# Kernel optimization log

Measured on AMD Instinct MI355X. Metric: run time of the kernel, lower is better.

## Reference

```python
import jax, jax.numpy as jnp
import numpy as np
import math

B, H, W = 8, 512, 1024
BOUNDARY_WIDTH = 4
BOUNDARY_ITERATION = 4
KERNEL_SIZE = 7
DILATION_SIZE = 6
NEG = -1e30  # geodesic border for morphological dilation (kornia border_type='geodesic')
POS = 1e30   # geodesic border for erosion
DN = ('NCHW', 'OIHW', 'NCHW')


def _gaussian_kernel():
    size, sigma = 7, 1.0
    g = np.fromfunction(
        lambda x, y: 1.0 / (2 * math.pi * sigma ** 2)
        * math.e ** (-(((x - (size - 1) / 2) ** 2 + (y - (size - 1) / 2) ** 2) / (2 * sigma ** 2))),
        (size, size))
    g = g / g.sum()
    return jnp.asarray(g, jnp.float32)[None, None]  # [1,1,7,7]


def _cross_dilate(x):
    # morphological dilation with 3x3 cross structuring element (generate_binary_structure(2,1))
    p = jnp.pad(x, ((0, 0), (0, 0), (1, 1), (1, 1)), constant_values=NEG)
    c = p[..., 1:-1, 1:-1]
    return jnp.maximum(
        jnp.maximum(jnp.maximum(c, p[..., :-2, 1:-1]), p[..., 2:, 1:-1]),
        jnp.maximum(p[..., 1:-1, :-2], p[..., 1:-1, 2:]))


def _erode3(x):
    # morphological erosion with full 3x3 ones structuring element, geodesic border
    return jax.lax.reduce_window(x, jnp.float32(POS), jax.lax.min,
                                 (1, 1, 3, 3), (1, 1, 1, 1),
                                 [(0, 0), (0, 0), (1, 1), (1, 1)])


def _conv3_sum(x):
    # 3x3 all-ones conv (first_conv), VALID on already-padded input
    k = jnp.ones((1, 1, 3, 3), x.dtype)
    return jax.lax.conv_general_dilated(x, k, (1, 1), 'VALID', dimension_numbers=DN)


def _forward(x, prediction):
    lab = prediction.astype(jnp.float32)
    # boundaries where dilated labels differ from eroded labels
    boundaries = (_cross_dilate(lab) != _erode3(lab)).astype(jnp.float32)
    out = x
    diff = BOUNDARY_WIDTH // BOUNDARY_ITERATION
    for it in range(BOUNDARY_ITERATION):
        prev = out
        r = 0 if (BOUNDARY_WIDTH == 0 or it == BOUNDARY_ITERATION - 1) else BOUNDARY_WIDTH - diff * it - 1
        eb = boundaries
        for _ in range(r):  # dilation by diamond of radius r == r cross-dilations
            eb = _cross_dilate(eb)
        mask = (eb == 0).astype(jnp.float32)  # non-boundary mask
        xm = out * mask
        xp = jnp.pad(xm, ((0, 0), (0, 0), (1, 1), (1, 1)), mode='edge')       # ReplicationPad2d(1)
        mp = jnp.pad(mask, ((0, 0), (0, 0), (1, 1), (1, 1)), mode='edge')
        y = _conv3_sum(xp)
        n = _conv3_sum(mp).astype(jnp.int32)  # .long() truncation; values are exact small ints
        n_safe = jnp.where(n == 0, 1, n).astype(y.dtype)
        avg = jnp.where(n == 0, prev, y / n_safe)
        out = jnp.where(mask == 0, avg, prev)
    # dilated gaussian smoothing: ReplicationPad2d(18) + 7x7 conv, dilation 6
    pad = DILATION_SIZE * 3
    op = jnp.pad(out, ((0, 0), (0, 0), (pad, pad), (pad, pad)), mode='edge')
    out = jax.lax.conv_general_dilated(op, _gaussian_kernel(), (1, 1), 'VALID',
                                       rhs_dilation=(DILATION_SIZE, DILATION_SIZE),
                                       dimension_numbers=DN)
    return out


def setup_inputs() -> dict:
    key = jax.random.key(0)
    k1, k2 = jax.random.split(key)
    x = jax.random.normal(k1, (B, 1, H, W), dtype=jnp.float32)
    prediction = jax.random.randint(k2, (B, 1, H, W), 0, 19, dtype=jnp.int32)
    return {"x": x, "prediction": prediction}


def reference(x, prediction):
    return _forward(x, prediction)
```

## Files before the change

### kernel.cpp

```cpp
#include <hip/hip_runtime.h>

#define B_ 8
#define H_ 512
#define W_ 1024
#define NPX (B_*H_*W_)

#define TILE 32
#define HD 4
#define RD 40
#define HB 7
#define RB 46
#define HP 8
#define RP 48

__device__ __forceinline__ int clampi(int v, int lo, int hi) {
    return v < lo ? lo : (v > hi ? hi : v);
}
__device__ __forceinline__ int imax(int a, int b) { return a > b ? a : b; }
__device__ __forceinline__ int imin(int a, int b) { return a < b ? a : b; }

__global__ __launch_bounds__(256)
void bsws_stage1(const float* __restrict__ xg, const int* __restrict__ predg,
                 float* __restrict__ outg)
{
    __shared__ int sPred[RP * RP];
    __shared__ unsigned long long sB[4][RB];
    __shared__ int sFlag;
    __shared__ float sA[RD * RD];
    __shared__ float sC[RD * RD];
    __shared__ float sHX[RD * RD];
    __shared__ float sHM[RD * RD];

    const int tid = threadIdx.x;
    const int x0 = blockIdx.x * TILE;
    const int y0 = blockIdx.y * TILE;
    const size_t plane = (size_t)H_ * W_;
    const int*   pp = predg + blockIdx.z * plane;
    const float* xp = xg    + blockIdx.z * plane;
    float*       op = outg  + blockIdx.z * plane;

    const bool leftB  = (x0 == 0), rightB = (x0 + TILE == W_);
    const bool topB   = (y0 == 0), botB   = (y0 + TILE == H_);
    const bool borderB = leftB || rightB || topB || botB;

    if (!borderB) {
        for (int i = tid; i < (RP * RP) / 4; i += 256) {
            int ry = i / (RP / 4);
            int c4 = i - ry * (RP / 4);
            int gy = y0 - HP + ry;
            int4 v = *(const int4*)(pp + (size_t)gy * W_ + (x0 - HP) + 4 * c4);
            *(int4*)&sPred[ry * RP + 4 * c4] = v;
        }
    } else {
        for (int i = tid; i < RP * RP; i += 256) {
            int ry = i / RP, rx = i - ry * RP;
            int gy = y0 - HP + ry, gx = x0 - HP + rx;
            sPred[i] = (gy >= 0 && gy < H_ && gx >= 0 && gx < W_) ? pp[(size_t)gy * W_ + gx] : -1;
        }
    }
    __syncthreads();

    {
        const int lane = tid & 63, wv = tid >> 6;
        for (int row = wv; row < RB; row += 4) {
            bool pred = false;
            if (lane < RB) {
                const int py = row + 1, px = lane + 1;
                int c = sPred[py * RP + px];
                if (c >= 0) {
                    int up = sPred[(py - 1) * RP + px];
                    int dn = sPred[(py + 1) * RP + px];
                    int lf = sPred[py * RP + px - 1];
                    int rt = sPred[py * RP + px + 1];
                    int ul = sPred[(py - 1) * RP + px - 1];
                    int ur = sPred[(py - 1) * RP + px + 1];
                    int dl = sPred[(py + 1) * RP + px - 1];
                    int dr = sPred[(py + 1) * RP + px + 1];
                    int mx = imax(imax(up, dn), imax(lf, rt));
                    int Bv = 0x7fffffff;
                    int mn = imin(imin(imin(up < 0 ? Bv : up, dn < 0 ? Bv : dn),
                                       imin(lf < 0 ? Bv : lf, rt < 0 ? Bv : rt)),
                                  imin(imin(ul < 0 ? Bv : ul, ur < 0 ? Bv : ur),
                                       imin(dl < 0 ? Bv : dl, dr < 0 ? Bv : dr)));
                    pred = (mx > c) || (mn < c);
                }
            }
            unsigned long long bal = __ballot(pred);
            if (lane == 0) sB[0][row] = bal;
        }
    }
    __syncthreads();

    if (tid < 64) {
        bool ok = true;
        if (tid < RB) {
            int gy = y0 - HB + tid;
            if (gy >= 0 && gy < H_) {
                int jlo = leftB ? HB : 0;
                int jhi = rightB ? (RB - 1 - HB) : (RB - 1);
                unsigned long long vmask = (((1ULL << (jhi - jlo + 1)) - 1ULL) << jlo);
                ok = ((sB[0][tid] & vmask) == vmask);
            }
        }
        unsigned long long all = __ballot(ok);
        if (tid == 0) sFlag = (all == ~0ULL) ? 1 : 0;
    }
    __syncthreads();

    if (sFlag) {
        int ty = tid >> 3, tx4 = (tid & 7) * 4;
        const float4 v = *(const float4*)(xp + (size_t)(y0 + ty) * W_ + (x0 + tx4));
        *(float4*)(op + (size_t)(y0 + ty) * W_ + (x0 + tx4)) = v;
        return;
    }

    for (int i = tid; i < RD * RD; i += 256) {
        int ry = i / RD, rx = i - ry * RD;
        int gy = clampi(y0 - HD + ry, 0, H_ - 1);
        int gx = clampi(x0 - HD + rx, 0, W_ - 1);
        sA[i] = xp[(size_t)gy * W_ + gx];
    }

    #pragma unroll
    for (int lvl = 1; lvl < 4; ++lvl) {
        __syncthreads();
        if (tid < RB) {
            unsigned long long c = sB[lvl - 1][tid];
            unsigned long long u = (tid > 0)      ? sB[lvl - 1][tid - 1] : 0ULL;
            unsigned long long d = (tid < RB - 1) ? sB[lvl - 1][tid + 1] : 0ULL;
            sB[lvl][tid] = c | (c << 1) | (c >> 1) | u | d;
        }
    }
    __syncthreads();

    if (borderB) {
        const bool act = tid < 4 * RB;
        unsigned long long val = 0; int lvl = 0, row = 0;
        if (act) {
            lvl = tid / RB; row = tid - lvl * RB;
            int srcRow = clampi(row, topB ? HB : 0, botB ? (RB - 1 - HB) : RB - 1);
            val = sB[lvl][srcRow];
            if (leftB) {
                unsigned long long b = (val >> HB) & 1ULL;
                unsigned long long lo = (1ULL << HB) - 1;
                val = (val & ~lo) | (b ? lo : 0ULL);
            }
            if (rightB) {
                const int jb = RB - 1 - HB;
                unsigned long long b = (val >> jb) & 1ULL;
                unsigned long long keep = (1ULL << (jb + 1)) - 1;
                unsigned long long hi = (((1ULL << RB) - 1) & ~keep);
                val = (val & keep) | (b ? hi : 0ULL);
            }
        }
        __syncthreads();
        if (act) sB[lvl][row] = val;
    }
    __syncthreads();

    float* cur = sA;
    float* nxt = sC;
    #pragma unroll
    for (int it = 0; it < 4; ++it) {
        const int r = 3 - it;
        const unsigned long long* br = sB[r];

        for (int i = tid; i < RD * RD; i += 256) {
            int ry = i / RD, rx = i - ry * RD;
            unsigned long long row = br[ry + (HB - HD)];
            int rxm = rx > 0 ? rx - 1 : 0;
            int rxp = rx < RD - 1 ? rx + 1 : RD - 1;
            float m0 = ((row >> (rx + 2)) & 1ULL) ? 0.f : 1.f;
            float m1 = ((row >> (rx + 3)) & 1ULL) ? 0.f : 1.f;
            float m2 = ((row >> (rx + 4)) & 1ULL) ? 0.f : 1.f;
            float a0 = cur[ry * RD + rxm];
            float a1 = cur[ry * RD + rx];
            float a2 = cur[ry * RD + rxp];
            sHX[i] = m0 * a0 + m1 * a1 + m2 * a2;
            sHM[i] = m0 + m1 + m2;
        }
        __syncthreads();

        for (int i = tid; i < 38 * 38; i += 256) {
            int q = i / 38;
            int ry = 1 + q, rx = 1 + (i - q * 38);
            int idx = ry * RD + rx;
            float n = sHM[idx - RD] + sHM[idx] + sHM[idx + RD];
            float y = sHX[idx - RD] + sHX[idx] + sHX[idx + RD];
            float c = cur[idx];
            unsigned long long row = br[ry + (HB - HD)];
            bool masked = ((row >> (rx + 3)) & 1ULL) != 0ULL;
            float avg = y * __builtin_amdgcn_rcpf(n);
            nxt[idx] = (masked && n > 0.5f) ? avg : c;
        }
        __syncthreads();

        if (borderB) {
            for (int i = tid; i < RD * RD; i += 256) {
                int ry = i / RD, rx = i - ry * RD;
                int ryc = clampi(ry, topB ? HD : 0, botB ? (RD - 1 - HD) : RD - 1);
                int rxc = clampi(rx, leftB ? HD : 0, rightB ? (RD - 1 - HD) : RD - 1);
                if (ryc != ry || rxc != rx) nxt[i] = nxt[ryc * RD + rxc];
            }
        }
        __syncthreads();
        float* t = cur; cur = nxt; nxt = t;
    }

    for (int i = tid; i < TILE * TILE; i += 256) {
        int ty = i >> 5, tx = i & 31;
        op[(size_t)(y0 + ty) * W_ + (x0 + tx)] = cur[(ty + HD) * RD + (tx + HD)];
    }
}

#define GW0 0.39905027965f
#define GW1 0.24203622800f
#define GW2 0.05400558260f
#define GW3 0.00443304810f

__global__ __launch_bounds__(256)
void gaussH(const float* __restrict__ in, float* __restrict__ out)
{
    int idx = blockIdx.x * 256 + threadIdx.x;
    const float* row = in + (idx & ~(W_ - 1));
    int gx = idx & (W_ - 1);
    float acc = GW3 * (row[clampi(gx - 18, 0, W_ - 1)] + row[clampi(gx + 18, 0, W_ - 1)])
              + GW2 * (row[clampi(gx - 12, 0, W_ - 1)] + row[clampi(gx + 12, 0, W_ - 1)])
              + GW1 * (row[clampi(gx - 6,  0, W_ - 1)] + row[clampi(gx + 6,  0, W_ - 1)])
              + GW0 *  row[gx];
    out[idx] = acc;
}

__global__ __launch_bounds__(256)
void gaussV(const float* __restrict__ in, float* __restrict__ out)
{
    int idx = blockIdx.x * 256 + threadIdx.x;
    int gx = idx & (W_ - 1);
    int gy = (idx >> 10) & (H_ - 1);
    const float* pl = in + (size_t)(idx >> 19 << 19);
    float acc = GW3 * (pl[(clampi(gy - 18, 0, H_ - 1) << 10) | gx] + pl[(clampi(gy + 18, 0, H_ - 1) << 10) | gx])
              + GW2 * (pl[(clampi(gy - 12, 0, H_ - 1) << 10) | gx] + pl[(clampi(gy + 12, 0, H_ - 1) << 10) | gx])
              + GW1 * (pl[(clampi(gy - 6,  0, H_ - 1) << 10) | gx] + pl[(clampi(gy + 6,  0, H_ - 1) << 10) | gx])
              + GW0 *  pl[(gy << 10) | gx];
    out[idx] = acc;
}

#define GTW 64
#define GTH 64
#define GHALO 18
#define GRH (GTH + 2*GHALO)

__global__ __launch_bounds__(256)
void bsws_stage2_tiled(const float* __restrict__ ing, float* __restrict__ outg)
{
    __shared__ float sH[GRH][GTW];

    const int tid = threadIdx.x;
    const int x0 = blockIdx.x * GTW;
    const int y0 = blockIdx.y * GTH;
    const size_t plane = (size_t)H_ * W_;
    const float* ip = ing  + blockIdx.z * plane;
    float*       op = outg + blockIdx.z * plane;

    for (int i = tid; i < GRH * GTW; i += 256) {
        int row = i >> 6, col = i & 63;
        int gy = clampi(y0 - GHALO + row, 0, H_ - 1);
        const float* rowp = ip + (size_t)gy * W_;
        int gx = x0 + col;
        float acc = GW3 * (rowp[clampi(gx - 18, 0, W_ - 1)] + rowp[clampi(gx + 18, 0, W_ - 1)])
                  + GW2 * (rowp[clampi(gx - 12, 0, W_ - 1)] + rowp[clampi(gx + 12, 0, W_ - 1)])
                  + GW1 * (rowp[clampi(gx - 6,  0, W_ - 1)] + rowp[clampi(gx + 6,  0, W_ - 1)])
                  + GW0 *  rowp[gx];
        sH[row][col] = acc;
    }
    __syncthreads();

    for (int i = tid; i < GTH * GTW; i += 256) {
        int ty = i >> 6, tx = i & 63;
        float acc = GW3 * (sH[ty][tx]      + sH[ty + 36][tx])
                  + GW2 * (sH[ty + 6][tx]  + sH[ty + 30][tx])
                  + GW1 * (sH[ty + 12][tx] + sH[ty + 24][tx])
                  + GW0 *  sH[ty + 18][tx];
        op[(size_t)(y0 + ty) * W_ + (x0 + tx)] = acc;
    }
}

extern "C" void kernel_launch(void* const* d_in, const int* in_sizes, int n_in,
                              void* d_out, int out_size, void* d_ws, size_t ws_size,
                              hipStream_t stream) {
    const float* x    = (const float*)d_in[0];
    const int*   pred = (const int*)d_in[1];
    float*       out  = (float*)d_out;
    float*       mid  = (float*)d_ws;

    bsws_stage1<<<dim3(W_ / TILE, H_ / TILE, B_), dim3(256), 0, stream>>>(x, pred, mid);

    const size_t plane_bytes = (size_t)NPX * 4;
    if (ws_size >= 2 * plane_bytes) {
        float* midH = mid + NPX;
        gaussH<<<NPX / 256, 256, 0, stream>>>(mid, midH);
        gaussV<<<NPX / 256, 256, 0, stream>>>(midH, out);
    } else {
        bsws_stage2_tiled<<<dim3(W_ / GTW, H_ / GTH, B_), dim3(256), 0, stream>>>(mid, out);
    }
}
```

Baseline: 122.5 us.

## Precompute boundary bitmap in separate kernel and vectorize Gaussian passes

Adds a pre-pass kernel that computes a per-pixel boundary bitmap with ballots, so the main stage can decide early whether a tile is fully boundary and take the copy-through path before loading its label halo. Shared memory is reduced by aliasing the label buffer with the horizontal scratch buffers. The separable Gaussian kernels are rewritten to process one row per block with float4 loads and stores. This adds an extra kernel launch and a full read of the labels in exchange for cheaper early exit and wider memory accesses.

```diff
diff --git a/kernel.cpp b/kernel.cpp
--- a/kernel.cpp
+++ b/kernel.cpp
@@ -20,16 +20,64 @@
 __device__ __forceinline__ int imin(int a, int b) { return a < b ? a : b; }
 
 __global__ __launch_bounds__(256)
-void bsws_stage1(const float* __restrict__ xg, const int* __restrict__ predg,
-                 float* __restrict__ outg)
-{
-    __shared__ int sPred[RP * RP];
+void k_flags(const int* __restrict__ pred, unsigned long long* __restrict__ bmap)
+{
+    const int tid = threadIdx.x;
+    const int idx = blockIdx.x * 256 + tid;
+    const int gx   = idx & (W_ - 1);
+    const int grow = idx >> 10;
+    const int yi   = grow & (H_ - 1);
+    const int rup  = (yi == 0)      ? grow : grow - 1;
+    const int rdn  = (yi == H_ - 1) ? grow : grow + 1;
+
+    const int c = pred[(size_t)grow * W_ + gx];
+    const int u = pred[(size_t)rup  * W_ + gx];
+    const int d = pred[(size_t)rdn  * W_ + gx];
+    const int vmax = imax(c, imax(u, d));
+    int       vmin = imin(c, imin(u, d));
+
+    const int lane = tid & 63;
+    int cL = __shfl_up(c, 1);
+    int vL = __shfl_up(vmin, 1);
+    int cR = __shfl_down(c, 1);
+    int vR = __shfl_down(vmin, 1);
+    if (lane == 0) {
+        if (gx > 0) {
+            cL = pred[(size_t)grow * W_ + gx - 1];
+            int u2 = pred[(size_t)rup * W_ + gx - 1];
+            int d2 = pred[(size_t)rdn * W_ + gx - 1];
+            vL = imin(cL, imin(u2, d2));
+        } else { cL = c; vL = vmin; }
+    }
+    if (lane == 63) {
+        if (gx < W_ - 1) {
+            cR = pred[(size_t)grow * W_ + gx + 1];
+            int u2 = pred[(size_t)rup * W_ + gx + 1];
+            int d2 = pred[(size_t)rdn * W_ + gx + 1];
+            vR = imin(cR, imin(u2, d2));
+        } else { cR = c; vR = vmin; }
+    }
+    const int mx = imax(vmax, imax(cL, cR));
+    const int mn = imin(vmin, imin(vL, vR));
+    const bool boundary = (mx > c) || (mn < c);
+    unsigned long long bal = __ballot(boundary);
+    if (lane == 0) bmap[idx >> 6] = bal;
+}
+
+__global__ __launch_bounds__(256)
+void k_stage1(const float* __restrict__ xg, const int* __restrict__ predg,
+              const unsigned long long* __restrict__ bmap, int use_bmap,
+              float* __restrict__ outg)
+{
+    __shared__ int sFlag;
+    __shared__ int sScratch[3200];
     __shared__ unsigned long long sB[4][RB];
-    __shared__ int sFlag;
     __shared__ float sA[RD * RD];
     __shared__ float sC[RD * RD];
-    __shared__ float sHX[RD * RD];
-    __shared__ float sHM[RD * RD];
+
+    int*   sPred = sScratch;
+    float* sHX = (float*)sScratch;
+    float* sHM = (float*)sScratch + RD * RD;
 
     const int tid = threadIdx.x;
     const int x0 = blockIdx.x * TILE;
@@ -39,31 +87,59 @@
     const float* xp = xg    + blockIdx.z * plane;
     float*       op = outg  + blockIdx.z * plane;
 
+    if (tid < 64) {
+        bool ok = (use_bmap != 0);
+        if (ok) {
+            const int rlo = (y0 > 0) ? y0 - 1 : 0;
+            const int rhi = (y0 + TILE < H_) ? y0 + TILE : H_ - 1;
+            const int row = rlo + tid;
+            if (row <= rhi) {
+                const int clo = (x0 > 0) ? x0 - 1 : 0;
+                const int chi = (x0 + TILE < W_) ? x0 + TILE : W_ - 1;
+                const unsigned long long* rb = bmap + ((size_t)blockIdx.z * H_ + row) * (W_ / 64);
+                const int w0 = clo >> 6, w1 = chi >> 6;
+                for (int w = w0; w <= w1; ++w) {
+                    int lo = (clo > (w << 6)) ? (clo - (w << 6)) : 0;
+                    int hi = (chi < ((w << 6) + 63)) ? (chi - (w << 6)) : 63;
+                    unsigned long long m = (lo == 0 && hi == 63) ? ~0ULL
+                                         : ((((1ULL << (hi - lo + 1)) - 1ULL) << lo));
+                    if ((rb[w] & m) != m) ok = false;
+                }
+            }
+        }
+        unsigned long long all = __ballot(ok);
+        if (tid == 0) sFlag = (all == ~0ULL) ? 1 : 0;
+    }
+    __syncthreads();
+
+    if (sFlag) {
+        int ty = tid >> 3, tx4 = (tid & 7) * 4;
+        const float4 v = *(const float4*)(xp + (size_t)(y0 + ty) * W_ + (x0 + tx4));
+        *(float4*)(op + (size_t)(y0 + ty) * W_ + (x0 + tx4)) = v;
+        return;
+    }
+
     const bool leftB  = (x0 == 0), rightB = (x0 + TILE == W_);
     const bool topB   = (y0 == 0), botB   = (y0 + TILE == H_);
     const bool borderB = leftB || rightB || topB || botB;
 
-    if (!borderB) {
-        for (int i = tid; i < (RP * RP) / 4; i += 256) {
-            int ry = i / (RP / 4);
-            int c4 = i - ry * (RP / 4);
-            int gy = y0 - HP + ry;
-            int4 v = *(const int4*)(pp + (size_t)gy * W_ + (x0 - HP) + 4 * c4);
-            *(int4*)&sPred[ry * RP + 4 * c4] = v;
-        }
-    } else {
-        for (int i = tid; i < RP * RP; i += 256) {
-            int ry = i / RP, rx = i - ry * RP;
-            int gy = y0 - HP + ry, gx = x0 - HP + rx;
-            sPred[i] = (gy >= 0 && gy < H_ && gx >= 0 && gx < W_) ? pp[(size_t)gy * W_ + gx] : -1;
-        }
+    for (int i = tid; i < RP * RP; i += 256) {
+        int ry = i / RP, rx = i - ry * RP;
+        int gy = y0 - HP + ry, gx = x0 - HP + rx;
+        sPred[i] = (gy >= 0 && gy < H_ && gx >= 0 && gx < W_) ? pp[(size_t)gy * W_ + gx] : -1;
+    }
+    for (int i = tid; i < RD * RD; i += 256) {
+        int ry = i / RD, rx = i - ry * RD;
+        int gy = clampi(y0 - HD + ry, 0, H_ - 1);
+        int gx = clampi(x0 - HD + rx, 0, W_ - 1);
+        sA[i] = xp[(size_t)gy * W_ + gx];
     }
     __syncthreads();
 
     {
         const int lane = tid & 63, wv = tid >> 6;
         for (int row = wv; row < RB; row += 4) {
-            bool pred = false;
+            bool bp = false;
             if (lane < RB) {
                 const int py = row + 1, px = lane + 1;
                 int c = sPred[py * RP + px];
@@ -82,43 +158,12 @@
                                        imin(lf < 0 ? Bv : lf, rt < 0 ? Bv : rt)),
                                   imin(imin(ul < 0 ? Bv : ul, ur < 0 ? Bv : ur),
                                        imin(dl < 0 ? Bv : dl, dr < 0 ? Bv : dr)));
-                    pred = (mx > c) || (mn < c);
+                    bp = (mx > c) || (mn < c);
                 }
             }
-            unsigned long long bal = __ballot(pred);
+            unsigned long long bal = __ballot(bp);
             if (lane == 0) sB[0][row] = bal;
         }
-    }
-    __syncthreads();
-
-    if (tid < 64) {
-        bool ok = true;
-        if (tid < RB) {
-            int gy = y0 - HB + tid;
-            if (gy >= 0 && gy < H_) {
-                int jlo = leftB ? HB : 0;
-                int jhi = rightB ? (RB - 1 - HB) : (RB - 1);
-                unsigned long long vmask = (((1ULL << (jhi - jlo + 1)) - 1ULL) << jlo);
-                ok = ((sB[0][tid] & vmask) == vmask);
-            }
-        }
-        unsigned long long all = __ballot(ok);
-        if (tid == 0) sFlag = (all == ~0ULL) ? 1 : 0;
-    }
-    __syncthreads();
-
-    if (sFlag) {
-        int ty = tid >> 3, tx4 = (tid & 7) * 4;
-        const float4 v = *(const float4*)(xp + (size_t)(y0 + ty) * W_ + (x0 + tx4));
-        *(float4*)(op + (size_t)(y0 + ty) * W_ + (x0 + tx4)) = v;
-        return;
-    }
-
-    for (int i = tid; i < RD * RD; i += 256) {
-        int ry = i / RD, rx = i - ry * RD;
-        int gy = clampi(y0 - HD + ry, 0, H_ - 1);
-        int gx = clampi(x0 - HD + rx, 0, W_ - 1);
-        sA[i] = xp[(size_t)gy * W_ + gx];
     }
 
     #pragma unroll
@@ -221,28 +266,63 @@
 __global__ __launch_bounds__(256)
 void gaussH(const float* __restrict__ in, float* __restrict__ out)
 {
-    int idx = blockIdx.x * 256 + threadIdx.x;
-    const float* row = in + (idx & ~(W_ - 1));
-    int gx = idx & (W_ - 1);
-    float acc = GW3 * (row[clampi(gx - 18, 0, W_ - 1)] + row[clampi(gx + 18, 0, W_ - 1)])
-              + GW2 * (row[clampi(gx - 12, 0, W_ - 1)] + row[clampi(gx + 12, 0, W_ - 1)])
-              + GW1 * (row[clampi(gx - 6,  0, W_ - 1)] + row[clampi(gx + 6,  0, W_ - 1)])
-              + GW0 *  row[gx];
-    out[idx] = acc;
+    const int tid = threadIdx.x;
+    const float* rp = in  + (size_t)blockIdx.x * W_;
+    float*       wp = out + (size_t)blockIdx.x * W_;
+    const int gx0 = tid * 4;
+
+    float4 o;
+    if (tid >= 5 && tid <= 250) {
+        const float4* vp = (const float4*)(rp + gx0 - 20);
+        float4 fm5 = vp[0], fm4 = vp[1], fm3 = vp[2], fm2 = vp[3], fm1 = vp[4];
+        float4 f0 = vp[5], f1 = vp[6], f2 = vp[7], f3 = vp[8], f4 = vp[9], f5 = vp[10];
+        o.x = GW0 * f0.x + GW1 * (fm2.z + f1.z) + GW2 * (fm3.x + f3.x) + GW3 * (fm5.z + f4.z);
+        o.y = GW0 * f0.y + GW1 * (fm2.w + f1.w) + GW2 * (fm3.y + f3.y) + GW3 * (fm5.w + f4.w);
+        o.z = GW0 * f0.z + GW1 * (fm1.x + f2.x) + GW2 * (fm3.z + f3.z) + GW3 * (fm4.x + f5.x);
+        o.w = GW0 * f0.w + GW1 * (fm1.y + f2.y) + GW2 * (fm3.w + f3.w) + GW3 * (fm4.y + f5.y);
+    } else {
+        float r[4];
+        #pragma unroll
+        for (int j = 0; j < 4; ++j) {
+            int gx = gx0 + j;
+            r[j] = GW3 * (rp[clampi(gx - 18, 0, W_ - 1)] + rp[clampi(gx + 18, 0, W_ - 1)])
+                 + GW2 * (rp[clampi(gx - 12, 0, W_ - 1)] + rp[clampi(gx + 12, 0, W_ - 1)])
+                 + GW1 * (rp[clampi(gx - 6,  0, W_ - 1)] + rp[clampi(gx + 6,  0, W_ - 1)])
+                 + GW0 *  rp[gx];
+        }
+        o.x = r[0]; o.y = r[1]; o.z = r[2]; o.w = r[3];
+    }
+    *(float4*)(wp + gx0) = o;
 }
 
 __global__ __launch_bounds__(256)
 void gaussV(const float* __restrict__ in, float* __restrict__ out)
 {
-    int idx = blockIdx.x * 256 + threadIdx.x;
-    int gx = idx & (W_ - 1);
-    int gy = (idx >> 10) & (H_ - 1);
-    const float* pl = in + (size_t)(idx >> 19 << 19);
-    float acc = GW3 * (pl[(clampi(gy - 18, 0, H_ - 1) << 10) | gx] + pl[(clampi(gy + 18, 0, H_ - 1) << 10) | gx])
-              + GW2 * (pl[(clampi(gy - 12, 0, H_ - 1) << 10) | gx] + pl[(clampi(gy + 12, 0, H_ - 1) << 10) | gx])
-              + GW1 * (pl[(clampi(gy - 6,  0, H_ - 1) << 10) | gx] + pl[(clampi(gy + 6,  0, H_ - 1) << 10) | gx])
-              + GW0 *  pl[(gy << 10) | gx];
-    out[idx] = acc;
+    const int tid = threadIdx.x;
+    const int y   = blockIdx.x & (H_ - 1);
+    const int img = blockIdx.x >> 9;
+    const float* pl = in  + (size_t)img * H_ * W_;
+    float*       wp = out + (size_t)blockIdx.x * W_;
+    const int gx0 = tid * 4;
+
+    const float* r0 = pl + (size_t)clampi(y - 18, 0, H_ - 1) * W_ + gx0;
+    const float* r1 = pl + (size_t)clampi(y - 12, 0, H_ - 1) * W_ + gx0;
+    const float* r2 = pl + (size_t)clampi(y - 6,  0, H_ - 1) * W_ + gx0;
+    const float* r3 = pl + (size_t)y * W_ + gx0;
+    const float* r4 = pl + (size_t)clampi(y + 6,  0, H_ - 1) * W_ + gx0;
+    const float* r5 = pl + (size_t)clampi(y + 12, 0, H_ - 1) * W_ + gx0;
+    const float* r6 = pl + (size_t)clampi(y + 18, 0, H_ - 1) * W_ + gx0;
+
+    float4 a0 = *(const float4*)r0, a1 = *(const float4*)r1, a2 = *(const float4*)r2;
+    float4 a3 = *(const float4*)r3, a4 = *(const float4*)r4, a5 = *(const float4*)r5;
+    float4 a6 = *(const float4*)r6;
+
+    float4 o;
+    o.x = GW3 * (a0.x + a6.x) + GW2 * (a1.x + a5.x) + GW1 * (a2.x + a4.x) + GW0 * a3.x;
+    o.y = GW3 * (a0.y + a6.y) + GW2 * (a1.y + a5.y) + GW1 * (a2.y + a4.y) + GW0 * a3.y;
+    o.z = GW3 * (a0.z + a6.z) + GW2 * (a1.z + a5.z) + GW1 * (a2.z + a4.z) + GW0 * a3.z;
+    o.w = GW3 * (a0.w + a6.w) + GW2 * (a1.w + a5.w) + GW1 * (a2.w + a4.w) + GW0 * a3.w;
+    *(float4*)(wp + gx0) = o;
 }
 
 #define GTW 64
@@ -254,7 +334,6 @@
 void bsws_stage2_tiled(const float* __restrict__ ing, float* __restrict__ outg)
 {
     __shared__ float sH[GRH][GTW];
-
     const int tid = threadIdx.x;
     const int x0 = blockIdx.x * GTW;
     const int y0 = blockIdx.y * GTH;
@@ -274,7 +353,6 @@
         sH[row][col] = acc;
     }
     __syncthreads();
-
     for (int i = tid; i < GTH * GTW; i += 256) {
         int ty = i >> 6, tx = i & 63;
         float acc = GW3 * (sH[ty][tx]      + sH[ty + 36][tx])
@@ -293,14 +371,23 @@
     float*       out  = (float*)d_out;
     float*       mid  = (float*)d_ws;
 
-    bsws_stage1<<<dim3(W_ / TILE, H_ / TILE, B_), dim3(256), 0, stream>>>(x, pred, mid);
-
     const size_t plane_bytes = (size_t)NPX * 4;
-    if (ws_size >= 2 * plane_bytes) {
+    const size_t bmap_bytes  = (size_t)NPX / 8;
+
+    if (ws_size >= 2 * plane_bytes + bmap_bytes) {
         float* midH = mid + NPX;
-        gaussH<<<NPX / 256, 256, 0, stream>>>(mid, midH);
-        gaussV<<<NPX / 256, 256, 0, stream>>>(midH, out);
+        unsigned long long* bmap = (unsigned long long*)((char*)d_ws + 2 * plane_bytes);
+        k_flags<<<NPX / 256, 256, 0, stream>>>(pred, bmap);
+        k_stage1<<<dim3(W_ / TILE, H_ / TILE, B_), dim3(256), 0, stream>>>(x, pred, bmap, 1, mid);
+        gaussH<<<B_ * H_, 256, 0, stream>>>(mid, midH);
+        gaussV<<<B_ * H_, 256, 0, stream>>>(midH, out);
+    } else if (ws_size >= 2 * plane_bytes) {
+        float* midH = mid + NPX;
+        k_stage1<<<dim3(W_ / TILE, H_ / TILE, B_), dim3(256), 0, stream>>>(x, pred, nullptr, 0, mid);
+        gaussH<<<B_ * H_, 256, 0, stream>>>(mid, midH);
+        gaussV<<<B_ * H_, 256, 0, stream>>>(midH, out);
     } else {
+        k_stage1<<<dim3(W_ / TILE, H_ / TILE, B_), dim3(256), 0, stream>>>(x, pred, nullptr, 0, mid);
         bsws_stage2_tiled<<<dim3(W_ / GTW, H_ / GTH, B_), dim3(256), 0, stream>>>(mid, out);
     }
 }
```

After: 129.8 us. +6.0%, slower.
